# Performance work log

Hardware: AMD Instinct MI355X
Metric: run time of the kernel (lower is better)

## Reference

```python
import jax, jax.numpy as jnp
import numpy as np
import math

D_MODEL = 1024
NUM_HEADS = 16
N_GROUP = 4
HEAD_DIM = D_MODEL // NUM_HEADS  # 64
KV_DIM = N_GROUP * HEAD_DIM      # 256
BS, SEQ = 2, 2048


def setup_inputs() -> dict:
    key = jax.random.key(0)
    ks = jax.random.split(key, 7)
    s = 0.02
    return {
        "h": jax.random.normal(ks[0], (BS, SEQ, D_MODEL), dtype=jnp.float32),
        "wq_w": jax.random.normal(ks[1], (D_MODEL, D_MODEL), dtype=jnp.float32) * s,
        "wq_b": jnp.zeros((D_MODEL,), dtype=jnp.float32),
        "wk_w": jax.random.normal(ks[2], (KV_DIM, D_MODEL), dtype=jnp.float32) * s,
        "wk_b": jnp.zeros((KV_DIM,), dtype=jnp.float32),
        "wv_w": jax.random.normal(ks[3], (KV_DIM, D_MODEL), dtype=jnp.float32) * s,
        "wv_b": jnp.zeros((KV_DIM,), dtype=jnp.float32),
    }


def reference(h, wq_w, wq_b, wk_w, wk_b, wv_w, wv_b):
    bs, seq, _ = h.shape
    rep = NUM_HEADS // N_GROUP  # heads per KV group

    # Linear projections (torch Linear: x @ W.T + b)
    q = h @ wq_w.T + wq_b                     # [bs, seq, d_model]
    k = h @ wk_w.T + wk_b                     # [bs, seq, kv_dim]
    v = h @ wv_w.T + wv_b                     # [bs, seq, kv_dim]

    q = q.reshape(bs, seq, NUM_HEADS, HEAD_DIM).transpose(0, 2, 1, 3)  # [b,H,s,d]
    k = k.reshape(bs, seq, N_GROUP, HEAD_DIM)                          # [b,s,G,d]
    v = v.reshape(bs, seq, N_GROUP, HEAD_DIM)
    # torch .repeat(1,1,1,rep).view(...,num_heads,head_dim) maps head h -> group h//rep,
    # identical to repeating each group `rep` times consecutively along the head axis.
    k = jnp.repeat(k, rep, axis=2).transpose(0, 2, 1, 3)               # [b,H,s,d]
    v = jnp.repeat(v, rep, axis=2).transpose(0, 2, 1, 3)               # [b,H,s,d]

    scores = jnp.einsum("bhqd,bhkd->bhqk", q, k) / math.sqrt(HEAD_DIM)
    attn = jax.nn.softmax(scores, axis=-1)
    out = jnp.einsum("bhqk,bhkd->bhqd", attn, v)                       # [b,H,s,d]
    out = out.transpose(0, 2, 1, 3).reshape(bs, seq, NUM_HEADS * HEAD_DIM)
    return out
```

## Files before the change

### kernel.cpp

```cpp
#include <hip/hip_runtime.h>

typedef _Float16 f16;
typedef _Float16 f16x8 __attribute__((ext_vector_type(8)));
typedef _Float16 f16x4 __attribute__((ext_vector_type(4)));
typedef __fp16  h16x2 __attribute__((ext_vector_type(2)));
typedef float f32x4 __attribute__((ext_vector_type(4)));

#define MFMA16(a, b, c)   __builtin_amdgcn_mfma_f32_16x16x32_f16((a), (b), (c), 0, 0, 0)
#define MFMA16K(a, b, c)  __builtin_amdgcn_mfma_f32_16x16x16f16((a), (b), (c), 0, 0, 0)

#define SEQ 2048
#define DMODEL 1024
#define NH 16
#define NG 4
#define PAD 76

__device__ __forceinline__ f16x8 cvt8(const float4 a, const float4 b) {
    f16x8 r;
    r[0] = (f16)a.x; r[1] = (f16)a.y; r[2] = (f16)a.z; r[3] = (f16)a.w;
    r[4] = (f16)b.x; r[5] = (f16)b.y; r[6] = (f16)b.z; r[7] = (f16)b.w;
    return r;
}

__device__ __forceinline__ void gl_lds16(f16* lds, const f16* g) {
    __builtin_amdgcn_global_load_lds(
        (const __attribute__((address_space(1))) void*)g,
        (__attribute__((address_space(3))) void*)lds, 16, 0, 0);
}

#define HN  (4096 * 1024)
#define WQN (1024 * 1024)
#define WKN (256 * 1024)
#define WVN (256 * 1024)
#define TOT8 ((HN + WQN + WKN + WVN) / 8)

__global__ __launch_bounds__(256) void cvt_kernel(const float* __restrict__ h,
                                                  const float* __restrict__ wq,
                                                  const float* __restrict__ wk,
                                                  const float* __restrict__ wv,
                                                  f16* __restrict__ h16,
                                                  f16* __restrict__ W16) {
    const int c = blockIdx.x * 256 + threadIdx.x;
    if (c >= TOT8) return;
    const size_t e = (size_t)c * 8;
    const float* src;
    f16* dst;
    if (e < HN) {
        src = h + e; dst = h16 + e;
    } else {
        const size_t e2 = e - HN;
        if (e2 < WQN)            src = wq + e2;
        else if (e2 < WQN + WKN) src = wk + (e2 - WQN);
        else                     src = wv + (e2 - WQN - WKN);
        dst = W16 + e2;
    }
    const float4 a = *(const float4*)src;
    const float4 b = *(const float4*)(src + 4);
    *(f16x8*)dst = cvt8(a, b);
}

__global__ __launch_bounds__(256, 3) void qkv_gemm16(const f16* __restrict__ A,
                                                     const f16* __restrict__ W,
                                                     const float* __restrict__ bq,
                                                     const float* __restrict__ bk,
                                                     const float* __restrict__ bv,
                                                     f16* __restrict__ Qb,
                                                     f16* __restrict__ Kb,
                                                     f16* __restrict__ Vtb,
                                                     float qscale) {
    __shared__ __align__(16) f16 As[2][64 * 32];
    __shared__ __align__(16) f16 Bs[2][128 * 32];

    const int tid  = threadIdx.x;
    const int lane = tid & 63;
    const int l15  = lane & 15;
    const int l4   = lane >> 4;
    const int wave = tid >> 6;
    const int wm   = (wave >> 1) * 32;
    const int wn   = (wave & 1) * 64;
    const int bx   = blockIdx.x;
    const int m0   = blockIdx.y * 64;
    const int n0g  = bx * 128;

    const f16* Ag = A + ((size_t)(m0 + (lane >> 2))) * 1024 + (lane & 3) * 8;
    const f16* Wg = W + ((size_t)(n0g + (lane >> 2))) * 1024 + (lane & 3) * 8;
    const size_t rstep = (size_t)16 * 1024;

    f32x4 acc[2][4];
#pragma unroll
    for (int i = 0; i < 2; i++)
#pragma unroll
        for (int j = 0; j < 4; j++) acc[i][j] = (f32x4)0.0f;

    gl_lds16(&As[0][wave * 512],        Ag + (size_t)wave * rstep);
    gl_lds16(&Bs[0][wave * 1024],       Wg + (size_t)(wave * 2) * rstep);
    gl_lds16(&Bs[0][wave * 1024 + 512], Wg + (size_t)(wave * 2 + 1) * rstep);

    int cur = 0;
    for (int k0 = 0; k0 < DMODEL; k0 += 32) {
        __syncthreads();
        if (k0 + 32 < DMODEL) {
            const int nxt = cur ^ 1;
            const int kn = k0 + 32;
            gl_lds16(&As[nxt][wave * 512],        Ag + (size_t)wave * rstep + kn);
            gl_lds16(&Bs[nxt][wave * 1024],       Wg + (size_t)(wave * 2) * rstep + kn);
            gl_lds16(&Bs[nxt][wave * 1024 + 512], Wg + (size_t)(wave * 2 + 1) * rstep + kn);
        }

        const f16* Ab = As[cur];
        const f16* Bb = Bs[cur];
        f16x8 af[2], bf[4];
#pragma unroll
        for (int i = 0; i < 2; i++)
            af[i] = *(const f16x8*)&Ab[(wm + i * 16 + l15) * 32 + l4 * 8];
#pragma unroll
        for (int j = 0; j < 4; j++)
            bf[j] = *(const f16x8*)&Bb[(wn + j * 16 + l15) * 32 + l4 * 8];
        __builtin_amdgcn_s_setprio(1);
#pragma unroll
        for (int i = 0; i < 2; i++)
#pragma unroll
            for (int j = 0; j < 4; j++)
                acc[i][j] = MFMA16(af[i], bf[j], acc[i][j]);
        __builtin_amdgcn_s_setprio(0);
        cur ^= 1;
    }

    const float* bias; f16* C; int N, n0; float osc; int vmode;
    if (bx < 8)       { bias = bq; C = Qb;  N = 1024; n0 = bx * 128;        osc = qscale; vmode = 0; }
    else if (bx < 10) { bias = bk; C = Kb;  N = 256;  n0 = (bx - 8) * 128;  osc = 1.0f;   vmode = 0; }
    else              { bias = bv; C = Vtb; N = 256;  n0 = (bx - 10) * 128; osc = 1.0f;   vmode = 1; }

#pragma unroll
    for (int i = 0; i < 2; i++) {
        const int mbase = m0 + wm + i * 16 + l4 * 4;
#pragma unroll
        for (int j = 0; j < 4; j++) {
            const int n  = n0 + wn + j * 16 + l15;
            const float bb = bias[n];
            if (vmode == 0) {
#pragma unroll
                for (int r = 0; r < 4; r++)
                    C[(size_t)(mbase + r) * N + n] = (f16)((acc[i][j][r] + bb) * osc);
            } else {
                f16x4 p;
#pragma unroll
                for (int r = 0; r < 4; r++)
                    p[r] = (f16)((acc[i][j][r] + bb) * osc);
                const int batch = mbase >> 11;
                const int s     = mbase & 2047;
                *(f16x4*)&C[((size_t)(batch * 256 + n)) * SEQ + s] = p;
            }
        }
    }
}

__global__ __launch_bounds__(256, 2) void attn_kernel(const f16* __restrict__ Q,
                                                      const f16* __restrict__ Kt,
                                                      const f16* __restrict__ Vt,
                                                      float* __restrict__ out) {
    __shared__ __align__(16) f16 Ks[2][64 * PAD];
    __shared__ __align__(16) f16 Vs[2][64 * PAD];

    const int tid  = threadIdx.x;
    const int lane = tid & 63;
    const int l15  = lane & 15;
    const int l4   = lane >> 4;
    const int wave = tid >> 6;
    const int b    = blockIdx.z;
    const int hh   = blockIdx.y;
    const int g    = hh >> 2;
    const int q0   = blockIdx.x * 128;
    const int qw   = wave * 32;

    f16x8 qf[2][2];
#pragma unroll
    for (int rg = 0; rg < 2; rg++)
#pragma unroll
        for (int kt = 0; kt < 2; kt++)
            qf[rg][kt] = *(const f16x8*)&Q[((size_t)(b * SEQ + q0 + qw + rg * 16 + l15)) * DMODEL
                                           + hh * 64 + kt * 32 + l4 * 8];

    f32x4 oacc[2][4];
    f32x4 lacc[2];
    const f16x4 ones = {(f16)1.0f, (f16)1.0f, (f16)1.0f, (f16)1.0f};
#pragma unroll
    for (int rg = 0; rg < 2; rg++) {
        lacc[rg] = (f32x4)0.0f;
#pragma unroll
        for (int dt = 0; dt < 4; dt++) oacc[rg][dt] = (f32x4)0.0f;
    }

    const int srow = tid >> 2;
    const int sc8  = (tid & 3) * 8;
    const f16* Kg = Kt + (size_t)(b * SEQ + srow) * 256 + g * 64 + sc8;
    const f16* Vg = Vt + (size_t)(b * 256 + g * 64 + srow) * SEQ + sc8;

    {
        const f16x8 k0 = *(const f16x8*)(Kg);
        const f16x8 k1 = *(const f16x8*)(Kg + 32);
        const f16x8 v0 = *(const f16x8*)(Vg);
        const f16x8 v1 = *(const f16x8*)(Vg + 32);
        *(f16x8*)&Ks[0][srow * PAD + sc8]      = k0;
        *(f16x8*)&Ks[0][srow * PAD + 32 + sc8] = k1;
        *(f16x8*)&Vs[0][srow * PAD + sc8]      = v0;
        *(f16x8*)&Vs[0][srow * PAD + 32 + sc8] = v1;
    }
    __syncthreads();

    f16x4 pap[2][4];
    f16x4 vfp[4][4];

    int cur = 0;
    for (int t = 0; t < 32; t++) {
        const int kb   = t * 64;
        const bool more = t < 31;

        f16x8 rk0, rk1, rv0, rv1;
        if (more) {
            rk0 = *(const f16x8*)(Kg + (size_t)(kb + 64) * 256);
            rk1 = *(const f16x8*)(Kg + (size_t)(kb + 64) * 256 + 32);
            rv0 = *(const f16x8*)(Vg + kb + 64);
            rv1 = *(const f16x8*)(Vg + kb + 64 + 32);
        }

        if (t > 0) {
#pragma unroll
            for (int jt = 0; jt < 4; jt++)
#pragma unroll
                for (int dt = 0; dt < 4; dt++) {
                    oacc[0][dt] = MFMA16K(pap[0][jt], vfp[jt][dt], oacc[0][dt]);
                    oacc[1][dt] = MFMA16K(pap[1][jt], vfp[jt][dt], oacc[1][dt]);
                }
        }

        f32x4 sacc[2][4];
#pragma unroll
        for (int rg = 0; rg < 2; rg++)
#pragma unroll
            for (int jt = 0; jt < 4; jt++) sacc[rg][jt] = (f32x4)0.0f;
#pragma unroll
        for (int jt = 0; jt < 4; jt++) {
            const f16x8 kf0 = *(const f16x8*)&Ks[cur][(jt * 16 + l15) * PAD + l4 * 8];
            const f16x8 kf1 = *(const f16x8*)&Ks[cur][(jt * 16 + l15) * PAD + 32 + l4 * 8];
#pragma unroll
            for (int rg = 0; rg < 2; rg++) {
                sacc[rg][jt] = MFMA16(kf0, qf[rg][0], sacc[rg][jt]);
                sacc[rg][jt] = MFMA16(kf1, qf[rg][1], sacc[rg][jt]);
            }
        }

#pragma unroll
        for (int rg = 0; rg < 2; rg++)
#pragma unroll
            for (int jt = 0; jt < 4; jt++) {
                const float p0 = exp2f(fminf(sacc[rg][jt][0], 14.0f));
                const float p1 = exp2f(fminf(sacc[rg][jt][1], 14.0f));
                const float p2 = exp2f(fminf(sacc[rg][jt][2], 14.0f));
                const float p3 = exp2f(fminf(sacc[rg][jt][3], 14.0f));
                union { f16x4 v4; h16x2 v2[2]; } u;
                u.v2[0] = __builtin_amdgcn_cvt_pkrtz(p0, p1);
                u.v2[1] = __builtin_amdgcn_cvt_pkrtz(p2, p3);
                pap[rg][jt] = u.v4;
            }

#pragma unroll
        for (int jt = 0; jt < 4; jt++) {
            lacc[0] = MFMA16K(pap[0][jt], ones, lacc[0]);
            lacc[1] = MFMA16K(pap[1][jt], ones, lacc[1]);
        }

#pragma unroll
        for (int jt = 0; jt < 4; jt++)
#pragma unroll
            for (int dt = 0; dt < 4; dt++)
                vfp[jt][dt] = *(const f16x4*)&Vs[cur][(dt * 16 + l15) * PAD + jt * 16 + l4 * 4];

        if (more) {
            const int nxt = cur ^ 1;
            *(f16x8*)&Ks[nxt][srow * PAD + sc8]      = rk0;
            *(f16x8*)&Ks[nxt][srow * PAD + 32 + sc8] = rk1;
            *(f16x8*)&Vs[nxt][srow * PAD + sc8]      = rv0;
            *(f16x8*)&Vs[nxt][srow * PAD + 32 + sc8] = rv1;
        }
        __syncthreads();
        cur ^= 1;
    }

#pragma unroll
    for (int jt = 0; jt < 4; jt++)
#pragma unroll
        for (int dt = 0; dt < 4; dt++) {
            oacc[0][dt] = MFMA16K(pap[0][jt], vfp[jt][dt], oacc[0][dt]);
            oacc[1][dt] = MFMA16K(pap[1][jt], vfp[jt][dt], oacc[1][dt]);
        }

#pragma unroll
    for (int rg = 0; rg < 2; rg++)
#pragma unroll
        for (int r = 0; r < 4; r++) {
            const float inv = 1.0f / lacc[rg][r];
            const int q = q0 + qw + rg * 16 + l4 * 4 + r;
            float* op = out + ((size_t)(b * SEQ + q)) * DMODEL + hh * 64;
#pragma unroll
            for (int dt = 0; dt < 4; dt++)
                op[dt * 16 + l15] = oacc[rg][dt][r] * inv;
        }
}

extern "C" void kernel_launch(void* const* d_in, const int* in_sizes, int n_in,
                              void* d_out, int out_size, void* d_ws, size_t ws_size,
                              hipStream_t stream) {
    const float* h    = (const float*)d_in[0];
    const float* wq_w = (const float*)d_in[1];
    const float* wq_b = (const float*)d_in[2];
    const float* wk_w = (const float*)d_in[3];
    const float* wk_b = (const float*)d_in[4];
    const float* wv_w = (const float*)d_in[5];
    const float* wv_b = (const float*)d_in[6];
    float* out = (float*)d_out;

    char* ws = (char*)d_ws;
    f16* Qb  = (f16*)(ws + 0);
    f16* Kb  = (f16*)(ws + 8388608);
    f16* Vtb = (f16*)(ws + 10485760);
    f16* h16 = (f16*)(ws + 12582912);
    f16* W16 = (f16*)(ws + 20971520);

    const float qscale = 0.125f * 1.4426950408889634f;

    cvt_kernel<<<dim3(TOT8 / 256), 256, 0, stream>>>(h, wq_w, wk_w, wv_w, h16, W16);
    qkv_gemm16<<<dim3(12, 64), 256, 0, stream>>>(h16, W16, wq_b, wk_b, wv_b,
                                                 Qb, Kb, Vtb, qscale);
    attn_kernel<<<dim3(16, 16, 2), 256, 0, stream>>>(Qb, Kb, Vtb, out);
}
```

Measured before the change: 169.9 us.

## Halve attention query tile per block to double grid and raise occupancy

Reduces each attention block from 128 to 64 query rows, with each wave handling one 16-row group instead of two. This doubles the grid to 1024 blocks and raises launch bounds to 4 blocks per CU, aiming to fill more waves and hide memory latency. In exchange, each K/V tile staged in LDS is reused by half as many query rows, doubling K/V load traffic per unit of output.

```diff
diff --git a/kernel.cpp b/kernel.cpp
--- a/kernel.cpp
+++ b/kernel.cpp
@@ -155,7 +155,7 @@
     }
 }
 
-__global__ __launch_bounds__(256, 2) void attn_kernel(const f16* __restrict__ Q,
+__global__ __launch_bounds__(256, 4) void attn_kernel(const f16* __restrict__ Q,
                                                       const f16* __restrict__ Kt,
                                                       const f16* __restrict__ Vt,
                                                       float* __restrict__ out) {
@@ -170,26 +170,21 @@
     const int b    = blockIdx.z;
     const int hh   = blockIdx.y;
     const int g    = hh >> 2;
-    const int q0   = blockIdx.x * 128;
-    const int qw   = wave * 32;
-
-    f16x8 qf[2][2];
-#pragma unroll
-    for (int rg = 0; rg < 2; rg++)
-#pragma unroll
-        for (int kt = 0; kt < 2; kt++)
-            qf[rg][kt] = *(const f16x8*)&Q[((size_t)(b * SEQ + q0 + qw + rg * 16 + l15)) * DMODEL
-                                           + hh * 64 + kt * 32 + l4 * 8];
-
-    f32x4 oacc[2][4];
-    f32x4 lacc[2];
+    const int q0   = blockIdx.x * 64;
+    const int qw   = wave * 16;
+
+    f16x8 qf[2];
+#pragma unroll
+    for (int kt = 0; kt < 2; kt++)
+        qf[kt] = *(const f16x8*)&Q[((size_t)(b * SEQ + q0 + qw + l15)) * DMODEL
+                                   + hh * 64 + kt * 32 + l4 * 8];
+
+    f32x4 oacc[4];
+    f32x4 lacc;
     const f16x4 ones = {(f16)1.0f, (f16)1.0f, (f16)1.0f, (f16)1.0f};
-#pragma unroll
-    for (int rg = 0; rg < 2; rg++) {
-        lacc[rg] = (f32x4)0.0f;
-#pragma unroll
-        for (int dt = 0; dt < 4; dt++) oacc[rg][dt] = (f32x4)0.0f;
-    }
+    lacc = (f32x4)0.0f;
+#pragma unroll
+    for (int dt = 0; dt < 4; dt++) oacc[dt] = (f32x4)0.0f;
 
     const int srow = tid >> 2;
     const int sc8  = (tid & 3) * 8;
@@ -208,7 +203,7 @@
     }
     __syncthreads();
 
-    f16x4 pap[2][4];
+    f16x4 pap[4];
     f16x4 vfp[4][4];
 
     int cur = 0;
@@ -228,47 +223,36 @@
 #pragma unroll
             for (int jt = 0; jt < 4; jt++)
 #pragma unroll
-                for (int dt = 0; dt < 4; dt++) {
-                    oacc[0][dt] = MFMA16K(pap[0][jt], vfp[jt][dt], oacc[0][dt]);
-                    oacc[1][dt] = MFMA16K(pap[1][jt], vfp[jt][dt], oacc[1][dt]);
-                }
-        }
-
-        f32x4 sacc[2][4];
-#pragma unroll
-        for (int rg = 0; rg < 2; rg++)
-#pragma unroll
-            for (int jt = 0; jt < 4; jt++) sacc[rg][jt] = (f32x4)0.0f;
+                for (int dt = 0; dt < 4; dt++)
+                    oacc[dt] = MFMA16K(pap[jt], vfp[jt][dt], oacc[dt]);
+        }
+
+        f32x4 sacc[4];
+#pragma unroll
+        for (int jt = 0; jt < 4; jt++) sacc[jt] = (f32x4)0.0f;
 #pragma unroll
         for (int jt = 0; jt < 4; jt++) {
             const f16x8 kf0 = *(const f16x8*)&Ks[cur][(jt * 16 + l15) * PAD + l4 * 8];
             const f16x8 kf1 = *(const f16x8*)&Ks[cur][(jt * 16 + l15) * PAD + 32 + l4 * 8];
-#pragma unroll
-            for (int rg = 0; rg < 2; rg++) {
-                sacc[rg][jt] = MFMA16(kf0, qf[rg][0], sacc[rg][jt]);
-                sacc[rg][jt] = MFMA16(kf1, qf[rg][1], sacc[rg][jt]);
-            }
-        }
-
-#pragma unroll
-        for (int rg = 0; rg < 2; rg++)
-#pragma unroll
-            for (int jt = 0; jt < 4; jt++) {
-                const float p0 = exp2f(fminf(sacc[rg][jt][0], 14.0f));
-                const float p1 = exp2f(fminf(sacc[rg][jt][1], 14.0f));
-                const float p2 = exp2f(fminf(sacc[rg][jt][2], 14.0f));
-                const float p3 = exp2f(fminf(sacc[rg][jt][3], 14.0f));
-                union { f16x4 v4; h16x2 v2[2]; } u;
-                u.v2[0] = __builtin_amdgcn_cvt_pkrtz(p0, p1);
-                u.v2[1] = __builtin_amdgcn_cvt_pkrtz(p2, p3);
-                pap[rg][jt] = u.v4;
-            }
+            sacc[jt] = MFMA16(kf0, qf[0], sacc[jt]);
+            sacc[jt] = MFMA16(kf1, qf[1], sacc[jt]);
+        }
 
 #pragma unroll
         for (int jt = 0; jt < 4; jt++) {
-            lacc[0] = MFMA16K(pap[0][jt], ones, lacc[0]);
-            lacc[1] = MFMA16K(pap[1][jt], ones, lacc[1]);
-        }
+            const float p0 = exp2f(fminf(sacc[jt][0], 14.0f));
+            const float p1 = exp2f(fminf(sacc[jt][1], 14.0f));
+            const float p2 = exp2f(fminf(sacc[jt][2], 14.0f));
+            const float p3 = exp2f(fminf(sacc[jt][3], 14.0f));
+            union { f16x4 v4; h16x2 v2[2]; } u;
+            u.v2[0] = __builtin_amdgcn_cvt_pkrtz(p0, p1);
+            u.v2[1] = __builtin_amdgcn_cvt_pkrtz(p2, p3);
+            pap[jt] = u.v4;
+        }
+
+#pragma unroll
+        for (int jt = 0; jt < 4; jt++)
+            lacc = MFMA16K(pap[jt], ones, lacc);
 
 #pragma unroll
         for (int jt = 0; jt < 4; jt++)
@@ -290,22 +274,18 @@
 #pragma unroll
     for (int jt = 0; jt < 4; jt++)
 #pragma unroll
-        for (int dt = 0; dt < 4; dt++) {
-            oacc[0][dt] = MFMA16K(pap[0][jt], vfp[jt][dt], oacc[0][dt]);
-            oacc[1][dt] = MFMA16K(pap[1][jt], vfp[jt][dt], oacc[1][dt]);
-        }
-
-#pragma unroll
-    for (int rg = 0; rg < 2; rg++)
-#pragma unroll
-        for (int r = 0; r < 4; r++) {
-            const float inv = 1.0f / lacc[rg][r];
-            const int q = q0 + qw + rg * 16 + l4 * 4 + r;
-            float* op = out + ((size_t)(b * SEQ + q)) * DMODEL + hh * 64;
-#pragma unroll
-            for (int dt = 0; dt < 4; dt++)
-                op[dt * 16 + l15] = oacc[rg][dt][r] * inv;
-        }
+        for (int dt = 0; dt < 4; dt++)
+            oacc[dt] = MFMA16K(pap[jt], vfp[jt][dt], oacc[dt]);
+
+#pragma unroll
+    for (int r = 0; r < 4; r++) {
+        const float inv = 1.0f / lacc[r];
+        const int q = q0 + qw + l4 * 4 + r;
+        float* op = out + ((size_t)(b * SEQ + q)) * DMODEL + hh * 64;
+#pragma unroll
+        for (int dt = 0; dt < 4; dt++)
+            op[dt * 16 + l15] = oacc[dt][r] * inv;
+    }
 }
 
 extern "C" void kernel_launch(void* const* d_in, const int* in_sizes, int n_in,
@@ -332,5 +312,5 @@
     cvt_kernel<<<dim3(TOT8 / 256), 256, 0, stream>>>(h, wq_w, wk_w, wv_w, h16, W16);
     qkv_gemm16<<<dim3(12, 64), 256, 0, stream>>>(h16, W16, wq_b, wk_b, wv_b,
                                                  Qb, Kb, Vtb, qscale);
-    attn_kernel<<<dim3(16, 16, 2), 256, 0, stream>>>(Qb, Kb, Vtb, out);
-}
+    attn_kernel<<<dim3(32, 16, 2), 256, 0, stream>>>(Qb, Kb, Vtb, out);
+}
```

After: 177.7 us. 1.05x slower.
